# Kernel optimization log

Hardware: AMD Instinct MI355X
Metric: run time of the kernel (lower is better)

## Reference

```python
import jax, jax.numpy as jnp
import numpy as np

V, F = 100000, 200000
N, H, W, K = 4, 512, 512, 4
SIGMA = 1e-4
GAMMA = 1e-4
BG = (1.0, 1.0, 1.0)
EPS = 1e-10
ZNEAR, ZFAR = 1.0, 100.0


def setup_inputs() -> dict:
    key = jax.random.key(0)
    ks = jax.random.split(key, 7)
    verts = jax.random.normal(ks[0], (V, 3), dtype=jnp.float32)
    vn = jax.random.normal(ks[1], (V, 3), dtype=jnp.float32)
    vertex_normals = vn / jnp.maximum(jnp.linalg.norm(vn, axis=-1, keepdims=True), 1e-12)
    bc = jax.random.uniform(ks[2], (N, H, W, K, 3), dtype=jnp.float32) + 1e-3
    bary_coords = bc / jnp.sum(bc, axis=-1, keepdims=True)
    # signed pixel-to-face distances, small scale comparable to sigma
    dists = jax.random.normal(ks[3], (N, H, W, K), dtype=jnp.float32) * 1e-4
    zbuf = jax.random.uniform(ks[4], (N, H, W, K), minval=ZNEAR, maxval=ZFAR, dtype=jnp.float32)
    faces = jax.random.randint(ks[5], (F, 3), 0, V, dtype=jnp.int64 if jax.config.jax_enable_x64 else jnp.int32)
    # include -1 entries (empty pixels), as produced by the rasterizer
    pix_to_face = jax.random.randint(ks[6], (N, H, W, K), -1, F, dtype=jnp.int64 if jax.config.jax_enable_x64 else jnp.int32)
    return {"verts": verts, "vertex_normals": vertex_normals, "bary_coords": bary_coords,
            "dists": dists, "zbuf": zbuf, "faces": faces, "pix_to_face": pix_to_face}


def reference(verts, vertex_normals, bary_coords, dists, zbuf, faces, pix_to_face):
    dtype = bary_coords.dtype
    # --- NormalCalcuate: gather per-face vertex normals and interpolate ---
    faces_normals = vertex_normals[faces]                      # [F, 3, 3]
    valid = pix_to_face >= 0                                   # [N,H,W,K]
    idx = jnp.where(valid, pix_to_face, 0)
    attrs = faces_normals[idx]                                 # [N,H,W,K,3(verts),3(ch)]
    pixel_normals = jnp.einsum('nhwkv,nhwkvc->nhwkc', bary_coords, attrs)
    pixel_normals = jnp.where(valid[..., None], pixel_normals, jnp.zeros((), dtype))
    # --- softmax_rgb_blend (rgb part only) ---
    maskf = valid.astype(dtype)
    prob = jax.nn.sigmoid(-dists / SIGMA) * maskf              # coverage weights
    z_inv = (ZFAR - zbuf) / (ZFAR - ZNEAR) * maskf
    z_inv_max = jnp.maximum(jnp.max(z_inv, axis=-1, keepdims=True), EPS)
    w_num = prob * jnp.exp((z_inv - z_inv_max) / GAMMA)        # [N,H,W,K]
    delta = jnp.maximum(jnp.exp((EPS - z_inv_max) / GAMMA), EPS)  # [N,H,W,1]
    denom = jnp.sum(w_num, axis=-1, keepdims=True) + delta
    bg = jnp.asarray(BG, dtype)
    rgb = (jnp.einsum('nhwk,nhwkc->nhwc', w_num, pixel_normals) + delta * bg) / denom
    # --- F.normalize(dim=3) ---
    norm = jnp.maximum(jnp.linalg.norm(rgb, axis=-1, keepdims=True), 1e-12)
    return rgb / norm
```

## Files before the change

kernel.cpp:

```cpp
#include <hip/hip_runtime.h>
#include <hip/hip_bf16.h>

namespace {
constexpr int N_ = 4, H_ = 512, W_ = 512, K_ = 4;
constexpr float SIGMA_ = 1e-4f;
constexpr float GAMMA_ = 1e-4f;
constexpr float EPS_   = 1e-10f;
constexpr float ZNEAR_ = 1.0f, ZFAR_ = 100.0f;

typedef float f32x4 __attribute__((ext_vector_type(4), aligned(4)));
typedef int   i32x4 __attribute__((ext_vector_type(4), aligned(4)));
}

__global__ __launch_bounds__(256) void normal_shader_kernel(
    const float* __restrict__ vnorm,
    const float* __restrict__ bary,
    const float* __restrict__ dists,
    const float* __restrict__ zbuf,
    const int*   __restrict__ faces,
    const int*   __restrict__ ptf,
    float*       __restrict__ out,
    int P)
{
    const int p = blockIdx.x * blockDim.x + threadIdx.x;
    if (p >= P) return;

    const i32x4 f4 = __builtin_nontemporal_load(reinterpret_cast<const i32x4*>(ptf) + p);
    const int fidx[4] = {f4.x, f4.y, f4.z, f4.w};

    const f32x4 dv = __builtin_nontemporal_load(reinterpret_cast<const f32x4*>(dists) + p);
    const f32x4 zv = __builtin_nontemporal_load(reinterpret_cast<const f32x4*>(zbuf) + p);
    const float d[4] = {dv.x, dv.y, dv.z, dv.w};
    const float z[4] = {zv.x, zv.y, zv.z, zv.w};

    float prob[4], zinv[4];
    float zmax = EPS_;
#pragma unroll
    for (int k = 0; k < K_; ++k) {
        const bool valid = fidx[k] >= 0;
        prob[k] = valid ? 1.0f / (1.0f + __expf(d[k] * (1.0f / SIGMA_))) : 0.0f;
        zinv[k] = valid ? (ZFAR_ - z[k]) * (1.0f / (ZFAR_ - ZNEAR_)) : 0.0f;
        zmax = fmaxf(zmax, zinv[k]);
    }
    const float delta = fmaxf(__expf((EPS_ - zmax) * (1.0f / GAMMA_)), EPS_);

    float wn[4];
#pragma unroll
    for (int k = 0; k < K_; ++k)
        wn[k] = prob[k] * __expf((zinv[k] - zmax) * (1.0f / GAMMA_));

    int cl[4];
#pragma unroll
    for (int k = 0; k < K_; ++k)
        cl[k] = (wn[k] != 0.0f) ? fidx[k] : 0;

    i32x4 fv[4];
#pragma unroll
    for (int k = 0; k < K_; ++k)
        fv[k] = *reinterpret_cast<const i32x4*>(faces + 3 * (size_t)cl[k]);

    const f32x4* bp = reinterpret_cast<const f32x4*>(bary + (size_t)p * 12);
    const f32x4 bA = __builtin_nontemporal_load(bp + 0);
    const f32x4 bB = __builtin_nontemporal_load(bp + 1);
    const f32x4 bC = __builtin_nontemporal_load(bp + 2);
    const float bb[12] = {bA.x, bA.y, bA.z, bA.w,
                          bB.x, bB.y, bB.z, bB.w,
                          bC.x, bC.y, bC.z, bC.w};

    f32x4 n0[4], n1[4], n2[4];
#pragma unroll
    for (int k = 0; k < K_; ++k) {
        n0[k] = *reinterpret_cast<const f32x4*>(vnorm + 3 * (size_t)fv[k].x);
        n1[k] = *reinterpret_cast<const f32x4*>(vnorm + 3 * (size_t)fv[k].y);
        n2[k] = *reinterpret_cast<const f32x4*>(vnorm + 3 * (size_t)fv[k].z);
    }

    float acc0 = 0.f, acc1 = 0.f, acc2 = 0.f, wsum = 0.f;
#pragma unroll
    for (int k = 0; k < K_; ++k) {
        wsum += wn[k];
        const float b0 = bb[3 * k + 0], b1 = bb[3 * k + 1], b2 = bb[3 * k + 2];
        acc0 += wn[k] * (b0 * n0[k].x + b1 * n1[k].x + b2 * n2[k].x);
        acc1 += wn[k] * (b0 * n0[k].y + b1 * n1[k].y + b2 * n2[k].y);
        acc2 += wn[k] * (b0 * n0[k].z + b1 * n1[k].z + b2 * n2[k].z);
    }

    const float inv_denom = 1.0f / (wsum + delta);
    const float r0 = (acc0 + delta) * inv_denom;
    const float r1 = (acc1 + delta) * inv_denom;
    const float r2 = (acc2 + delta) * inv_denom;
    const float nrm = fmaxf(sqrtf(r0 * r0 + r1 * r1 + r2 * r2), 1e-12f);
    const float inv = 1.0f / nrm;

    float* op = out + (size_t)p * 3;
    __builtin_nontemporal_store(r0 * inv, op + 0);
    __builtin_nontemporal_store(r1 * inv, op + 1);
    __builtin_nontemporal_store(r2 * inv, op + 2);
}

extern "C" void kernel_launch(void* const* d_in, const int* in_sizes, int n_in,
                              void* d_out, int out_size, void* d_ws, size_t ws_size,
                              hipStream_t stream) {
    const float* vnorm = (const float*)d_in[1];
    const float* bary  = (const float*)d_in[2];
    const float* dists = (const float*)d_in[3];
    const float* zbuf  = (const float*)d_in[4];
    const int*   faces = (const int*)d_in[5];
    const int*   ptf   = (const int*)d_in[6];
    float*       out   = (float*)d_out;

    const int P = N_ * H_ * W_;
    const dim3 block(256);
    const dim3 grid((P + block.x - 1) / block.x);
    hipLaunchKernelGGL(normal_shader_kernel, grid, block, 0, stream,
                       vnorm, bary, dists, zbuf, faces, ptf, out, P);
}
```

Baseline: 164.4 us.

## Precompute per-face vertex-normal table to remove dependent gathers

Adds a pre-pass kernel that gathers the three vertex normals of each face into a padded 64-byte row in workspace. The shading kernel then fetches one contiguous row per sample instead of a face-index lookup followed by three dependent vertex lookups. This removes a level of dependent memory latency and scattered accesses, at the cost of an extra launch and writing a table of about 12.8MB. A fused fallback without nontemporal hints is kept for when the workspace is too small, and the output store becomes a single 3-wide store.

```diff
diff --git a/kernel.cpp b/kernel.cpp
--- a/kernel.cpp
+++ b/kernel.cpp
@@ -3,6 +3,7 @@
 
 namespace {
 constexpr int N_ = 4, H_ = 512, W_ = 512, K_ = 4;
+constexpr int F_ = 200000, V_ = 100000;
 constexpr float SIGMA_ = 1e-4f;
 constexpr float GAMMA_ = 1e-4f;
 constexpr float EPS_   = 1e-10f;
@@ -10,9 +11,107 @@
 
 typedef float f32x4 __attribute__((ext_vector_type(4), aligned(4)));
 typedef int   i32x4 __attribute__((ext_vector_type(4), aligned(4)));
+typedef float f32x3 __attribute__((ext_vector_type(3), aligned(4)));
+}
+
+
+__global__ __launch_bounds__(256) void build_fnorm_kernel(
+    const float* __restrict__ vnorm,
+    const int*   __restrict__ faces,
+    float*       __restrict__ fnorm)
+{
+    const int f = blockIdx.x * blockDim.x + threadIdx.x;
+    if (f < F_) {
+        const i32x4 fv = *reinterpret_cast<const i32x4*>(faces + 3 * (size_t)f);
+        const f32x4 n0 = *reinterpret_cast<const f32x4*>(vnorm + 3 * (size_t)fv.x);
+        const f32x4 n1 = *reinterpret_cast<const f32x4*>(vnorm + 3 * (size_t)fv.y);
+        const f32x4 n2 = *reinterpret_cast<const f32x4*>(vnorm + 3 * (size_t)fv.z);
+        f32x4* row = reinterpret_cast<f32x4*>(fnorm + (size_t)f * 16);
+        __builtin_nontemporal_store(f32x4{n0.x, n0.y, n0.z, n1.x}, row + 0);
+        __builtin_nontemporal_store(f32x4{n1.y, n1.z, n2.x, n2.y}, row + 1);
+        __builtin_nontemporal_store(f32x4{n2.z, 0.f, 0.f, 0.f},    row + 2);
+    }
+    __threadfence();
 }
 
 __global__ __launch_bounds__(256) void normal_shader_kernel(
+    const float* __restrict__ fnorm,
+    const float* __restrict__ bary,
+    const float* __restrict__ dists,
+    const float* __restrict__ zbuf,
+    const int*   __restrict__ ptf,
+    float*       __restrict__ out,
+    int P)
+{
+    const int p = blockIdx.x * blockDim.x + threadIdx.x;
+    if (p >= P) return;
+
+    const i32x4 f4 = __builtin_nontemporal_load(reinterpret_cast<const i32x4*>(ptf) + p);
+    const int fidx[4] = {f4.x, f4.y, f4.z, f4.w};
+    const f32x4 dv = __builtin_nontemporal_load(reinterpret_cast<const f32x4*>(dists) + p);
+    const f32x4 zv = __builtin_nontemporal_load(reinterpret_cast<const f32x4*>(zbuf) + p);
+    const float d[4] = {dv.x, dv.y, dv.z, dv.w};
+    const float z[4] = {zv.x, zv.y, zv.z, zv.w};
+
+    float prob[4], zinv[4];
+    float zmax = EPS_;
+#pragma unroll
+    for (int k = 0; k < K_; ++k) {
+        const bool valid = fidx[k] >= 0;
+        prob[k] = valid ? 1.0f / (1.0f + __expf(d[k] * (1.0f / SIGMA_))) : 0.0f;
+        zinv[k] = valid ? (ZFAR_ - z[k]) * (1.0f / (ZFAR_ - ZNEAR_)) : 0.0f;
+        zmax = fmaxf(zmax, zinv[k]);
+    }
+    const float delta = fmaxf(__expf((EPS_ - zmax) * (1.0f / GAMMA_)), EPS_);
+
+    float wn[4];
+#pragma unroll
+    for (int k = 0; k < K_; ++k)
+        wn[k] = prob[k] * __expf((zinv[k] - zmax) * (1.0f / GAMMA_));
+
+    const float* rp[4];
+#pragma unroll
+    for (int k = 0; k < K_; ++k)
+        rp[k] = fnorm + ((size_t)((wn[k] != 0.0f) ? fidx[k] : 0) << 4);
+
+    f32x4 ra[4], rb[4], rc[4];
+#pragma unroll
+    for (int k = 0; k < K_; ++k) {
+        ra[k] = reinterpret_cast<const f32x4*>(rp[k])[0];
+        rb[k] = reinterpret_cast<const f32x4*>(rp[k])[1];
+        rc[k] = reinterpret_cast<const f32x4*>(rp[k])[2];
+    }
+
+    const f32x4* bp = reinterpret_cast<const f32x4*>(bary + (size_t)p * 12);
+    const f32x4 bA = __builtin_nontemporal_load(bp + 0);
+    const f32x4 bB = __builtin_nontemporal_load(bp + 1);
+    const f32x4 bC = __builtin_nontemporal_load(bp + 2);
+    const float bb[12] = {bA.x, bA.y, bA.z, bA.w,
+                          bB.x, bB.y, bB.z, bB.w,
+                          bC.x, bC.y, bC.z, bC.w};
+
+    float acc0 = 0.f, acc1 = 0.f, acc2 = 0.f, wsum = 0.f;
+#pragma unroll
+    for (int k = 0; k < K_; ++k) {
+        wsum += wn[k];
+        const float b0 = bb[3 * k + 0], b1 = bb[3 * k + 1], b2 = bb[3 * k + 2];
+        acc0 += wn[k] * (b0 * ra[k].x + b1 * ra[k].w + b2 * rb[k].z);
+        acc1 += wn[k] * (b0 * ra[k].y + b1 * rb[k].x + b2 * rb[k].w);
+        acc2 += wn[k] * (b0 * ra[k].z + b1 * rb[k].y + b2 * rc[k].x);
+    }
+
+    const float inv_denom = 1.0f / (wsum + delta);
+    const float r0 = (acc0 + delta) * inv_denom;
+    const float r1 = (acc1 + delta) * inv_denom;
+    const float r2 = (acc2 + delta) * inv_denom;
+    const float nrm = fmaxf(sqrtf(r0 * r0 + r1 * r1 + r2 * r2), 1e-12f);
+    const float inv = 1.0f / nrm;
+
+    __builtin_nontemporal_store(f32x3{r0 * inv, r1 * inv, r2 * inv},
+                                reinterpret_cast<f32x3*>(out + (size_t)p * 3));
+}
+
+__global__ __launch_bounds__(256) void normal_shader_fused_kernel(
     const float* __restrict__ vnorm,
     const float* __restrict__ bary,
     const float* __restrict__ dists,
@@ -24,17 +123,13 @@
 {
     const int p = blockIdx.x * blockDim.x + threadIdx.x;
     if (p >= P) return;
-
-    const i32x4 f4 = __builtin_nontemporal_load(reinterpret_cast<const i32x4*>(ptf) + p);
+    const i32x4 f4 = reinterpret_cast<const i32x4*>(ptf)[p];
     const int fidx[4] = {f4.x, f4.y, f4.z, f4.w};
-
-    const f32x4 dv = __builtin_nontemporal_load(reinterpret_cast<const f32x4*>(dists) + p);
-    const f32x4 zv = __builtin_nontemporal_load(reinterpret_cast<const f32x4*>(zbuf) + p);
+    const f32x4 dv = reinterpret_cast<const f32x4*>(dists)[p];
+    const f32x4 zv = reinterpret_cast<const f32x4*>(zbuf)[p];
     const float d[4] = {dv.x, dv.y, dv.z, dv.w};
     const float z[4] = {zv.x, zv.y, zv.z, zv.w};
-
-    float prob[4], zinv[4];
-    float zmax = EPS_;
+    float prob[4], zinv[4], zmax = EPS_;
 #pragma unroll
     for (int k = 0; k < K_; ++k) {
         const bool valid = fidx[k] >= 0;
@@ -43,30 +138,18 @@
         zmax = fmaxf(zmax, zinv[k]);
     }
     const float delta = fmaxf(__expf((EPS_ - zmax) * (1.0f / GAMMA_)), EPS_);
-
     float wn[4];
 #pragma unroll
-    for (int k = 0; k < K_; ++k)
-        wn[k] = prob[k] * __expf((zinv[k] - zmax) * (1.0f / GAMMA_));
-
+    for (int k = 0; k < K_; ++k) wn[k] = prob[k] * __expf((zinv[k] - zmax) * (1.0f / GAMMA_));
     int cl[4];
 #pragma unroll
-    for (int k = 0; k < K_; ++k)
-        cl[k] = (wn[k] != 0.0f) ? fidx[k] : 0;
-
+    for (int k = 0; k < K_; ++k) cl[k] = (wn[k] != 0.0f) ? fidx[k] : 0;
     i32x4 fv[4];
 #pragma unroll
-    for (int k = 0; k < K_; ++k)
-        fv[k] = *reinterpret_cast<const i32x4*>(faces + 3 * (size_t)cl[k]);
-
+    for (int k = 0; k < K_; ++k) fv[k] = *reinterpret_cast<const i32x4*>(faces + 3 * (size_t)cl[k]);
     const f32x4* bp = reinterpret_cast<const f32x4*>(bary + (size_t)p * 12);
-    const f32x4 bA = __builtin_nontemporal_load(bp + 0);
-    const f32x4 bB = __builtin_nontemporal_load(bp + 1);
-    const f32x4 bC = __builtin_nontemporal_load(bp + 2);
-    const float bb[12] = {bA.x, bA.y, bA.z, bA.w,
-                          bB.x, bB.y, bB.z, bB.w,
-                          bC.x, bC.y, bC.z, bC.w};
-
+    const f32x4 bA = bp[0], bB = bp[1], bC = bp[2];
+    const float bb[12] = {bA.x, bA.y, bA.z, bA.w, bB.x, bB.y, bB.z, bB.w, bC.x, bC.y, bC.z, bC.w};
     f32x4 n0[4], n1[4], n2[4];
 #pragma unroll
     for (int k = 0; k < K_; ++k) {
@@ -74,28 +157,23 @@
         n1[k] = *reinterpret_cast<const f32x4*>(vnorm + 3 * (size_t)fv[k].y);
         n2[k] = *reinterpret_cast<const f32x4*>(vnorm + 3 * (size_t)fv[k].z);
     }
-
     float acc0 = 0.f, acc1 = 0.f, acc2 = 0.f, wsum = 0.f;
 #pragma unroll
     for (int k = 0; k < K_; ++k) {
         wsum += wn[k];
-        const float b0 = bb[3 * k + 0], b1 = bb[3 * k + 1], b2 = bb[3 * k + 2];
+        const float b0 = bb[3 * k], b1 = bb[3 * k + 1], b2 = bb[3 * k + 2];
         acc0 += wn[k] * (b0 * n0[k].x + b1 * n1[k].x + b2 * n2[k].x);
         acc1 += wn[k] * (b0 * n0[k].y + b1 * n1[k].y + b2 * n2[k].y);
         acc2 += wn[k] * (b0 * n0[k].z + b1 * n1[k].z + b2 * n2[k].z);
     }
-
     const float inv_denom = 1.0f / (wsum + delta);
     const float r0 = (acc0 + delta) * inv_denom;
     const float r1 = (acc1 + delta) * inv_denom;
     const float r2 = (acc2 + delta) * inv_denom;
     const float nrm = fmaxf(sqrtf(r0 * r0 + r1 * r1 + r2 * r2), 1e-12f);
     const float inv = 1.0f / nrm;
-
     float* op = out + (size_t)p * 3;
-    __builtin_nontemporal_store(r0 * inv, op + 0);
-    __builtin_nontemporal_store(r1 * inv, op + 1);
-    __builtin_nontemporal_store(r2 * inv, op + 2);
+    op[0] = r0 * inv; op[1] = r1 * inv; op[2] = r2 * inv;
 }
 
 extern "C" void kernel_launch(void* const* d_in, const int* in_sizes, int n_in,
@@ -110,8 +188,19 @@
     float*       out   = (float*)d_out;
 
     const int P = N_ * H_ * W_;
-    const dim3 block(256);
-    const dim3 grid((P + block.x - 1) / block.x);
-    hipLaunchKernelGGL(normal_shader_kernel, grid, block, 0, stream,
-                       vnorm, bary, dists, zbuf, faces, ptf, out, P);
-}
+    const size_t table_bytes = (size_t)F_ * 16 * sizeof(float);
+
+    if (ws_size >= table_bytes) {
+        float* fnorm = (float*)d_ws;
+        hipLaunchKernelGGL(build_fnorm_kernel,
+                           dim3((F_ + 255) / 256), dim3(256), 0, stream,
+                           vnorm, faces, fnorm);
+        hipLaunchKernelGGL(normal_shader_kernel,
+                           dim3((P + 255) / 256), dim3(256), 0, stream,
+                           fnorm, bary, dists, zbuf, ptf, out, P);
+    } else {
+        hipLaunchKernelGGL(normal_shader_fused_kernel,
+                           dim3((P + 255) / 256), dim3(256), 0, stream,
+                           vnorm, bary, dists, zbuf, faces, ptf, out, P);
+    }
+}
```

New measurement: 303.1 us. 84.3% more time.
